# Performance work log

Measured on AMD Instinct MI355X. Metric: run time of the kernel, lower is better.

## Reference

```python
import jax, jax.numpy as jnp
import numpy as np

B, S, H, N = 2, 2048, 1024, 16
HN = H // N  # head dim = 64
EPS = 1e-12


def setup_inputs() -> dict:
    key = jax.random.key(0)
    ks = jax.random.split(key, 8)
    scale = 0.02
    return {
        "hidden_states": jax.random.normal(ks[0], (B, S, H), dtype=jnp.float32),
        "attention_mask": jnp.zeros((B, 1, 1, S), dtype=jnp.float32),
        "W_qkv": jax.random.normal(ks[1], (3 * H, H), dtype=jnp.float32) * scale,
        "b_qkv": jnp.zeros((3 * H,), dtype=jnp.float32),
        "W_out": jax.random.normal(ks[2], (H, H), dtype=jnp.float32) * scale,
        "b_out": jnp.zeros((H,), dtype=jnp.float32),
        "ln_gamma": jnp.ones((H,), dtype=jnp.float32),
        "ln_beta": jnp.zeros((H,), dtype=jnp.float32),
    }


def reference(hidden_states, attention_mask, W_qkv, b_qkv, W_out, b_out, ln_gamma, ln_beta):
    # QKV projection: torch Linear => x @ W.T + b
    qkv = jnp.einsum("bsh,oh->bso", hidden_states, W_qkv) + b_qkv  # [B,S,3H]
    q, k, v = jnp.split(qkv, 3, axis=-1)

    def heads(t):  # [B,S,H] -> [B,N,S,HN]
        return t.reshape(B, S, N, HN).transpose(0, 2, 1, 3)

    q, k, v = heads(q), heads(k), heads(v)
    nf = jnp.sqrt(jnp.sqrt(jnp.float32(HN)))
    scores = jnp.einsum("bnsd,bntd->bnst", q / nf, k / nf) + attention_mask  # [B,N,S,S]
    probs = jax.nn.softmax(scores, axis=-1)
    ctx = jnp.einsum("bnst,bntd->bnsd", probs, v)  # [B,N,S,HN]
    ctx = ctx.transpose(0, 2, 1, 3).reshape(B, S, H)

    # output dense + residual + LayerNorm
    out = jnp.einsum("bsh,oh->bso", ctx, W_out) + b_out
    x = out + hidden_states
    mean = jnp.mean(x, axis=-1, keepdims=True)
    var = jnp.mean(jnp.square(x - mean), axis=-1, keepdims=True)
    return (x - mean) * jax.lax.rsqrt(var + EPS) * ln_gamma + ln_beta
```

## Files before the change

### kernel.cpp

```cpp
#include <hip/hip_runtime.h>
#include <hip/hip_bf16.h>
#include <math.h>

#define Bq  2
#define Sq  2048
#define Hq  1024
#define Nq  16
#define HNq 64
#define Mq  (Bq*Sq)
#define H3q (3*Hq)

#define LOG2E 1.44269504088896340736f

typedef __attribute__((ext_vector_type(8))) short           short8;
typedef __attribute__((ext_vector_type(4))) short           short4s;
typedef __attribute__((ext_vector_type(8))) unsigned short  ushortx8;
typedef __attribute__((ext_vector_type(4))) unsigned short  ushortx4;
typedef __attribute__((ext_vector_type(4))) float           floatx4;

__device__ __forceinline__ unsigned short f2bf(float f) {
    union { float f; unsigned int u; } x; x.f = f;
    unsigned int r = (x.u + 0x7fffu + ((x.u >> 16) & 1u)) >> 16;
    return (unsigned short)r;
}

__device__ __forceinline__ unsigned int pkbf(float a, float b) {
    float2 t; t.x = a; t.y = b;
    __hip_bfloat162 h = __float22bfloat162_rn(t);
    union { __hip_bfloat162 h; unsigned int u; } c; c.h = h;
    return c.u;
}

__device__ __forceinline__ float bf2f(unsigned short v) {
    union { unsigned int u; float f; } x; x.u = (unsigned int)v << 16;
    return x.f;
}

__device__ __forceinline__ float fexp2(float x) {
    float r;
    asm("v_exp_f32 %0, %1" : "=v"(r) : "v"(x));
    return r;
}

__device__ __forceinline__ void gload16(const unsigned short* g, unsigned short* l) {
    __builtin_amdgcn_global_load_lds(
        (__attribute__((address_space(1))) void*)(unsigned long long)(g),
        (__attribute__((address_space(3))) void*)(unsigned int)(unsigned long long)(l),
        16, 0, 0);
}

__device__ __forceinline__ int swz(int r) { return (r ^ (r >> 2)) & 3; }

#define N_HID ((size_t)Mq * Hq)
#define N_HW  (N_HID + (size_t)H3q * Hq)
#define N_ALL (N_HW + (size_t)Hq * Hq)
#define CVT_BLKS ((int)(N_ALL / 2048))

__global__ __launch_bounds__(256) void cvt_all(
    const float* __restrict__ hidden, const float* __restrict__ wqkv,
    const float* __restrict__ wout, const float* __restrict__ mask,
    unsigned short* __restrict__ dst, unsigned short* __restrict__ em2)
{
    const int bid = blockIdx.x;
    if (bid >= CVT_BLKS) {
        const int t0   = ((bid - CVT_BLKS) * 256 + threadIdx.x) * 8;
        const int b    = t0 >> 11;
        const int t2   = t0 & 2047;
        const int kt   = t2 >> 6;
        const int t3   = t2 & 63;
        const int ks   = t3 >> 5;
        const int quad = (t3 >> 3) & 3;
        const int kb   = kt * 64 + ks * 32 + quad * 4;
        const float* mp = mask + (size_t)b * Sq + kb;
        float4 m0 = *(const float4*)(mp);
        float4 m1 = *(const float4*)(mp + 16);
        union { unsigned int u[4]; ushortx8 s; } o;
        o.u[0] = pkbf(fexp2(m0.x * LOG2E), fexp2(m0.y * LOG2E));
        o.u[1] = pkbf(fexp2(m0.z * LOG2E), fexp2(m0.w * LOG2E));
        o.u[2] = pkbf(fexp2(m1.x * LOG2E), fexp2(m1.y * LOG2E));
        o.u[3] = pkbf(fexp2(m1.z * LOG2E), fexp2(m1.w * LOG2E));
        *(ushortx8*)(em2 + t0) = o.s;
        return;
    }
    size_t i = ((size_t)bid * 256 + threadIdx.x) * 8;
    const float* src;
    if (i < N_HID)      src = hidden + i;
    else if (i < N_HW)  src = wqkv + (i - N_HID);
    else                src = wout + (i - N_HW);
    float4 a = *(const float4*)(src);
    float4 b = *(const float4*)(src + 4);
    union { unsigned int u[4]; ushortx8 s; } o;
    o.u[0] = pkbf(a.x, a.y); o.u[1] = pkbf(a.z, a.w);
    o.u[2] = pkbf(b.x, b.y); o.u[3] = pkbf(b.z, b.w);
    *(ushortx8*)(dst + i) = o.s;
}

#define TM 128
#define TN 128
#define TK 32

__global__ __launch_bounds__(256) void gemm_mfma_qkv(
    const unsigned short* __restrict__ A, const unsigned short* __restrict__ Bw,
    const float* __restrict__ bias, const float* __restrict__ mask,
    unsigned short* __restrict__ Qb, unsigned short* __restrict__ Kd,
    unsigned short* __restrict__ V5, int K)
{
    __shared__ unsigned short As[3][TM][TK];
    __shared__ unsigned short Bs[3][TN][TK];

    const int tid = threadIdx.x;
    const int w = tid >> 6, lane = tid & 63;
    const int l15 = lane & 15, quad = lane >> 4;
    const int wr = (w & 1) * 64;
    const int wc = (w >> 1) * 64;
    const int row0 = blockIdx.y * TM;
    const int col0 = blockIdx.x * TN;

    const int srow16 = lane >> 2;
    const int sgd    = lane & 3;
    const int sgsrc  = (sgd ^ swz(srow16)) * 8;

    floatx4 acc[4][4];
    #pragma unroll
    for (int i = 0; i < 4; i++)
        #pragma unroll
        for (int j = 0; j < 4; j++) acc[i][j] = (floatx4){0.f,0.f,0.f,0.f};

    const int aswz = swz(l15) * 8;
    const int NK = K / TK;

    #pragma unroll
    for (int t = 0; t < 2; t++) {
        #pragma unroll
        for (int c = 0; c < 2; c++) {
            int seg = w * 2 + c;
            int r = seg * 16 + srow16;
            gload16(A  + (size_t)(row0 + r) * K + t * TK + sgsrc, &As[t][seg * 16][0]);
            gload16(Bw + (size_t)(col0 + r) * K + t * TK + sgsrc, &Bs[t][seg * 16][0]);
        }
    }

    #pragma unroll 1
    for (int k = 0; k < NK; ++k) {
        if (k + 1 < NK) asm volatile("s_waitcnt vmcnt(4)" ::: "memory");
        else            asm volatile("s_waitcnt vmcnt(0)" ::: "memory");
        __builtin_amdgcn_s_barrier();
        __builtin_amdgcn_sched_barrier(0);

        const int cur = k % 3;
        if (k + 2 < NK) {
            const int nb  = (k + 2) % 3;
            const int k0n = (k + 2) * TK;
            #pragma unroll
            for (int c = 0; c < 2; c++) {
                int seg = w * 2 + c;
                int r = seg * 16 + srow16;
                gload16(A  + (size_t)(row0 + r) * K + k0n + sgsrc, &As[nb][seg * 16][0]);
                gload16(Bw + (size_t)(col0 + r) * K + k0n + sgsrc, &Bs[nb][seg * 16][0]);
            }
        }
        __builtin_amdgcn_sched_barrier(0);

        short8 af[4], bf[4];
        #pragma unroll
        for (int i = 0; i < 4; i++)
            af[i] = *(const short8*)&As[cur][wr + i * 16 + l15][(quad * 8) ^ aswz];
        #pragma unroll
        for (int j = 0; j < 4; j++)
            bf[j] = *(const short8*)&Bs[cur][wc + j * 16 + l15][(quad * 8) ^ aswz];
        __builtin_amdgcn_s_setprio(1);
        #pragma unroll
        for (int i = 0; i < 4; i++)
            #pragma unroll
            for (int j = 0; j < 4; j++)
                acc[i][j] = __builtin_amdgcn_mfma_f32_16x16x32_bf16(af[i], bf[j], acc[i][j], 0, 0, 0);
        __builtin_amdgcn_s_setprio(0);
    }

    const int cls = col0 >> 10;

    if (cls == 2) {
        #pragma unroll
        for (int i = 0; i < 4; i++) {
            const int rb = row0 + wr + i * 16 + quad * 4;
            const int b  = rb >> 11;
            const int s  = rb & (Sq - 1);
            const int kt32 = s >> 6;
            const int sw   = s & 63;
            const int kg   = sw >> 2;
            const int ks   = kg >> 3;
            const int q2   = kg & 3;
            const int hi   = (kg >> 2) & 1;
            float expm[4];
            #pragma unroll
            for (int rr = 0; rr < 4; rr++)
                expm[rr] = fexp2(mask[(size_t)b * Sq + s + rr] * LOG2E);
            #pragma unroll
            for (int j = 0; j < 4; j++) {
                const int c  = col0 + wc + j * 16 + l15;
                const int c2 = c - 2 * Hq;
                const int n  = c2 >> 6, d = c2 & 63;
                const int dt = d >> 4, dl = d & 15;
                const float bia = bias[c];
                ushortx4 o;
                #pragma unroll
                for (int rr = 0; rr < 4; rr++)
                    o[rr] = f2bf((acc[i][j][rr] + bia) * expm[rr]);
                const size_t off = (((size_t)(b * Nq + n) * 32 + kt32) << 12)
                                 + (size_t)((ks * 16 + dt * 4 + q2) * 128 + dl * 8 + hi * 4);
                *(ushortx4*)&V5[off] = o;
            }
        }
    } else {
        unsigned short* __restrict__ dst = (cls == 0) ? Qb : Kd;
        const int cshift = (cls == 0) ? 0 : Hq;
        const float qs = (cls == 0) ? (0.125f * LOG2E) : 1.0f;
        #pragma unroll
        for (int i = 0; i < 4; i++) {
            const int rb = row0 + wr + i * 16 + quad * 4;
            #pragma unroll
            for (int j = 0; j < 4; j++) {
                const int c = col0 + wc + j * 16 + l15;
                const float bia = bias[c];
                #pragma unroll
                for (int rr = 0; rr < 4; rr++)
                    dst[(size_t)(rb + rr) * Hq + (c - cshift)] =
                        f2bf((acc[i][j][rr] + bia) * qs);
            }
        }
    }
}

__global__ __launch_bounds__(256) void gemm_mfma_out(
    const unsigned short* __restrict__ A, const unsigned short* __restrict__ Bw,
    const float* __restrict__ bias, const float* __restrict__ res,
    unsigned short* __restrict__ X, int M, int Nd, int K)
{
    __shared__ unsigned short As[3][TM][TK];
    __shared__ unsigned short Bs[3][TN][TK];

    const int tid = threadIdx.x;
    const int w = tid >> 6, lane = tid & 63;
    const int l15 = lane & 15, quad = lane >> 4;
    const int wr = (w & 1) * 64;
    const int wc = (w >> 1) * 64;
    const int row0 = blockIdx.y * TM;
    const int col0 = blockIdx.x * TN;

    const int srow16 = lane >> 2;
    const int sgd    = lane & 3;
    const int sgsrc  = (sgd ^ swz(srow16)) * 8;

    floatx4 acc[4][4];
    #pragma unroll
    for (int i = 0; i < 4; i++)
        #pragma unroll
        for (int j = 0; j < 4; j++) acc[i][j] = (floatx4){0.f,0.f,0.f,0.f};

    const int aswz = swz(l15) * 8;
    const int NK = K / TK;

    #pragma unroll
    for (int t = 0; t < 2; t++) {
        #pragma unroll
        for (int c = 0; c < 2; c++) {
            int seg = w * 2 + c;
            int r = seg * 16 + srow16;
            gload16(A  + (size_t)(row0 + r) * K + t * TK + sgsrc, &As[t][seg * 16][0]);
            gload16(Bw + (size_t)(col0 + r) * K + t * TK + sgsrc, &Bs[t][seg * 16][0]);
        }
    }

    #pragma unroll 1
    for (int k = 0; k < NK; ++k) {
        if (k + 1 < NK) asm volatile("s_waitcnt vmcnt(4)" ::: "memory");
        else            asm volatile("s_waitcnt vmcnt(0)" ::: "memory");
        __builtin_amdgcn_s_barrier();
        __builtin_amdgcn_sched_barrier(0);

        const int cur = k % 3;
        if (k + 2 < NK) {
            const int nb  = (k + 2) % 3;
            const int k0n = (k + 2) * TK;
            #pragma unroll
            for (int c = 0; c < 2; c++) {
                int seg = w * 2 + c;
                int r = seg * 16 + srow16;
                gload16(A  + (size_t)(row0 + r) * K + k0n + sgsrc, &As[nb][seg * 16][0]);
                gload16(Bw + (size_t)(col0 + r) * K + k0n + sgsrc, &Bs[nb][seg * 16][0]);
            }
        }
        __builtin_amdgcn_sched_barrier(0);

        short8 af[4], bf[4];
        #pragma unroll
        for (int i = 0; i < 4; i++)
            af[i] = *(const short8*)&As[cur][wr + i * 16 + l15][(quad * 8) ^ aswz];
        #pragma unroll
        for (int j = 0; j < 4; j++)
            bf[j] = *(const short8*)&Bs[cur][wc + j * 16 + l15][(quad * 8) ^ aswz];
        __builtin_amdgcn_s_setprio(1);
        #pragma unroll
        for (int i = 0; i < 4; i++)
            #pragma unroll
            for (int j = 0; j < 4; j++)
                acc[i][j] = __builtin_amdgcn_mfma_f32_16x16x32_bf16(af[i], bf[j], acc[i][j], 0, 0, 0);
        __builtin_amdgcn_s_setprio(0);
    }

    #pragma unroll
    for (int i = 0; i < 4; i++) {
        const int rb = row0 + wr + i * 16 + quad * 4;
        #pragma unroll
        for (int j = 0; j < 4; j++) {
            const int c = col0 + wc + j * 16 + l15;
            const float bia = bias[c];
            #pragma unroll
            for (int rr = 0; rr < 4; rr++) {
                X[(size_t)(rb + rr) * Nd + c] =
                    f2bf(acc[i][j][rr] + bia + res[(size_t)(rb + rr) * Nd + c]);
            }
        }
    }
}

#define KTILES 16

__device__ __forceinline__ floatx4 mfma16(short8 a, short8 b, floatx4 c) {
    return __builtin_amdgcn_mfma_f32_16x16x32_bf16(a, b, c, 0, 0, 0);
}

__device__ __forceinline__ void do_lpv(
    const short8 (&pf0)[2], const short8 (&pf1)[2], const short8 (&mf)[2],
    const short8 (&vf)[8],
    floatx4 (&oacc0)[4], floatx4 (&oacc1)[4],
    floatx4 &lacc0, floatx4 &lacc1)
{
    __builtin_amdgcn_s_setprio(1);
    lacc0 = mfma16(mf[0], pf0[0], lacc0);
    lacc0 = mfma16(mf[1], pf0[1], lacc0);
    lacc1 = mfma16(mf[0], pf1[0], lacc1);
    lacc1 = mfma16(mf[1], pf1[1], lacc1);
    #pragma unroll
    for (int dt = 0; dt < 4; dt++) {
        oacc0[dt] = mfma16(vf[dt],     pf0[0], oacc0[dt]);
        oacc1[dt] = mfma16(vf[dt],     pf1[0], oacc1[dt]);
        oacc0[dt] = mfma16(vf[4 + dt], pf0[1], oacc0[dt]);
        oacc1[dt] = mfma16(vf[4 + dt], pf1[1], oacc1[dt]);
    }
    __builtin_amdgcn_s_setprio(0);
}

template<bool HAVER, bool PREF, int VWAIT>
__device__ __forceinline__ void attn_body(
    int kt,
    unsigned short (&KsL)[2][64][64],
    const unsigned short* kp, size_t kstep,
    const unsigned short* Vb, const unsigned short* e2b,
    int w, int l15, int quad,
    const short8 (&qf0)[2], const short8 (&qf1)[2],
    short8 (&vf)[8],
    const short8 (&pfR0)[2], const short8 (&pfR1)[2], const short8 (&mfR)[2],
    short8 (&pfW0)[2], short8 (&pfW1)[2], short8 (&mfW)[2],
    floatx4 (&oacc0)[4], floatx4 (&oacc1)[4],
    floatx4 &lacc0, floatx4 &lacc1)
{
    asm volatile("s_waitcnt vmcnt(%0)" :: "i"(VWAIT) : "memory");
    __builtin_amdgcn_s_barrier();
    __builtin_amdgcn_sched_barrier(0);

    const int cur = kt & 1;
    if (PREF) {
        const unsigned short* kpn = kp + (size_t)(kt + 1) * kstep;
        gload16(kpn,                  &KsL[cur ^ 1][w * 16][0]);
        gload16(kpn + (size_t)8 * Hq, &KsL[cur ^ 1][w * 16 + 8][0]);
    }
    __builtin_amdgcn_sched_barrier(0);

    const unsigned short* ep = e2b + kt * 64;
    mfW[0] = *(const short8*)(ep + quad * 8);
    mfW[1] = *(const short8*)(ep + 32 + quad * 8);

    floatx4 s0[4], s1[4];
    #pragma unroll
    for (int ct = 0; ct < 4; ct++) {
        s0[ct] = (floatx4){0.f,0.f,0.f,0.f};
        s1[ct] = (floatx4){0.f,0.f,0.f,0.f};
    }
    __builtin_amdgcn_s_setprio(1);
    #pragma unroll
    for (int ks = 0; ks < 2; ks++) {
        #pragma unroll
        for (int ct = 0; ct < 4; ct++) {
            short8 af = *(const short8*)&KsL[cur][ct * 16 + l15][((4 * ks + quad) ^ (l15 & 7)) * 8];
            s0[ct] = mfma16(af, qf0[ks], s0[ct]);
            s1[ct] = mfma16(af, qf1[ks], s1[ct]);
        }
    }
    __builtin_amdgcn_s_setprio(0);

    #pragma unroll
    for (int ks = 0; ks < 2; ks++) {
        union { unsigned int u[4]; short8 s; } pk;
        #pragma unroll
        for (int h = 0; h < 2; h++) {
            const int ct = ks * 2 + h;
            pk.u[h * 2]     = pkbf(fexp2(s0[ct][0]), fexp2(s0[ct][1]));
            pk.u[h * 2 + 1] = pkbf(fexp2(s0[ct][2]), fexp2(s0[ct][3]));
        }
        pfW0[ks] = pk.s;
    }
    #pragma unroll
    for (int ks = 0; ks < 2; ks++) {
        union { unsigned int u[4]; short8 s; } pk;
        #pragma unroll
        for (int h = 0; h < 2; h++) {
            const int ct = ks * 2 + h;
            pk.u[h * 2]     = pkbf(fexp2(s1[ct][0]), fexp2(s1[ct][1]));
            pk.u[h * 2 + 1] = pkbf(fexp2(s1[ct][2]), fexp2(s1[ct][3]));
        }
        pfW1[ks] = pk.s;
    }

    if (HAVER)
        do_lpv(pfR0, pfR1, mfR, vf, oacc0, oacc1, lacc0, lacc1);

    const unsigned short* vt = Vb + (size_t)kt * 4096 + quad * 128 + l15 * 8;
    vf[0] = *(const short8*)(vt);
    vf[1] = *(const short8*)(vt + 512);
    vf[2] = *(const short8*)(vt + 1024);
    vf[3] = *(const short8*)(vt + 1536);
    vf[4] = *(const short8*)(vt + 2048);
    vf[5] = *(const short8*)(vt + 2560);
    vf[6] = *(const short8*)(vt + 3072);
    vf[7] = *(const short8*)(vt + 3584);
}

__global__ __launch_bounds__(256) void attn_mfma(
    const unsigned short* __restrict__ Qb, const unsigned short* __restrict__ Kd,
    const unsigned short* __restrict__ V5, const unsigned short* __restrict__ em2,
    unsigned short* __restrict__ Opart, float* __restrict__ Lpart)
{
    __shared__ unsigned short Ks[2][64][64];

    const int tid  = threadIdx.x;
    const int w    = tid >> 6;
    const int lane = tid & 63;
    const int l15  = lane & 15;
    const int quad = lane >> 4;

    const int i_    = blockIdx.x;
    const int gl8   = i_ & 7;
    const int rest  = i_ >> 3;
    const int qtile = rest & 15;
    const int g     = (rest >> 4) * 8 + gl8;
    const int bn    = g >> 1;
    const int z     = g & 1;
    const int n     = bn & 15;
    const int b     = bn >> 4;

    const int kbase = z * (KTILES * 64);

    short8 qf0[2], qf1[2];
    {
        const int qrow0 = qtile * 128 + w * 16 + l15;
        const unsigned short* qp = Qb + (size_t)(b * Sq + qrow0) * Hq + n * HNq + quad * 8;
        qf0[0] = *(const short8*)(qp);
        qf0[1] = *(const short8*)(qp + 32);
        qp += (size_t)64 * Hq;
        qf1[0] = *(const short8*)(qp);
        qf1[1] = *(const short8*)(qp + 32);
    }

    floatx4 oacc0[4], oacc1[4];
    #pragma unroll
    for (int dt = 0; dt < 4; dt++) {
        oacc0[dt] = (floatx4){0.f,0.f,0.f,0.f};
        oacc1[dt] = (floatx4){0.f,0.f,0.f,0.f};
    }
    floatx4 lacc0 = (floatx4){0.f,0.f,0.f,0.f};
    floatx4 lacc1 = (floatx4){0.f,0.f,0.f,0.f};

    const int krow8 = lane >> 3;
    const int kgr   = (lane & 7) ^ (krow8 & 7);
    const unsigned short* kp = Kd + (size_t)(b * Sq + kbase + w * 16 + krow8) * Hq
                                  + n * HNq + kgr * 8;
    const size_t kstep = (size_t)64 * Hq;

    gload16(kp,                  &Ks[0][w * 16][0]);
    gload16(kp + (size_t)8 * Hq, &Ks[0][w * 16 + 8][0]);

    const unsigned short* Vb  = V5 + ((size_t)(b * Nq + n) * 32 + z * KTILES) * 4096;
    const unsigned short* e2b = em2 + (size_t)(b * 32 + z * KTILES) * 64;

    short8 vf[8];
    short8 pfA0[2], pfA1[2], mfA[2];
    short8 pfB0[2], pfB1[2], mfB[2];

    attn_body<false, true, 0>(0, Ks, kp, kstep, Vb, e2b, w, l15, quad,
        qf0, qf1, vf, pfB0, pfB1, mfB, pfA0, pfA1, mfA, oacc0, oacc1, lacc0, lacc1);

    #pragma unroll 1
    for (int kt = 1; kt < KTILES - 1; kt += 2) {
        attn_body<true, true, 10>(kt, Ks, kp, kstep, Vb, e2b, w, l15, quad,
            qf0, qf1, vf, pfA0, pfA1, mfA, pfB0, pfB1, mfB, oacc0, oacc1, lacc0, lacc1);
        attn_body<true, true, 10>(kt + 1, Ks, kp, kstep, Vb, e2b, w, l15, quad,
            qf0, qf1, vf, pfB0, pfB1, mfB, pfA0, pfA1, mfA, oacc0, oacc1, lacc0, lacc1);
    }
    attn_body<true, false, 10>(KTILES - 1, Ks, kp, kstep, Vb, e2b, w, l15, quad,
        qf0, qf1, vf, pfA0, pfA1, mfA, pfB0, pfB1, mfB, oacc0, oacc1, lacc0, lacc1);
    do_lpv(pfB0, pfB1, mfB, vf, oacc0, oacc1, lacc0, lacc1);

    unsigned short* Ow = Opart + (size_t)z * Mq * Hq;
    #pragma unroll
    for (int sub = 0; sub < 2; sub++) {
        const float l_i = sub ? lacc1[0] : lacc0[0];
        const int qrow = qtile * 128 + sub * 64 + w * 16 + l15;
        if (quad == 0)
            Lpart[(size_t)z * Mq * Nq + (size_t)(b * Sq + qrow) * Nq + n] = l_i;
        #pragma unroll
        for (int dt = 0; dt < 4; dt++) {
            const floatx4 oa = sub ? oacc1[dt] : oacc0[dt];
            union { unsigned int u[2]; ushortx4 s; } o;
            o.u[0] = pkbf(oa[0], oa[1]);
            o.u[1] = pkbf(oa[2], oa[3]);
            const int col = n * HNq + dt * 16 + quad * 4;
            *(ushortx4*)&Ow[(size_t)(b * Sq + qrow) * Hq + col] = o.s;
        }
    }
}

__global__ __launch_bounds__(256) void attn_merge(
    const unsigned short* __restrict__ Opart, const float* __restrict__ Lpart,
    unsigned short* __restrict__ ctx)
{
    const size_t idx = ((size_t)blockIdx.x * 256 + threadIdx.x) * 4;
    const int row = (int)(idx >> 10);
    const int n   = ((int)idx >> 6) & 15;
    const float l = Lpart[(size_t)row * Nq + n]
                  + Lpart[(size_t)Mq * Nq + (size_t)row * Nq + n];
    const float inv = 1.0f / l;
    ushortx4 a = *(const ushortx4*)(Opart + idx);
    ushortx4 c = *(const ushortx4*)(Opart + (size_t)Mq * Hq + idx);
    union { unsigned int u[2]; ushortx4 s; } o;
    o.u[0] = pkbf((bf2f(a[0]) + bf2f(c[0])) * inv, (bf2f(a[1]) + bf2f(c[1])) * inv);
    o.u[1] = pkbf((bf2f(a[2]) + bf2f(c[2])) * inv, (bf2f(a[3]) + bf2f(c[3])) * inv);
    *(ushortx4*)(ctx + idx) = o.s;
}

__global__ __launch_bounds__(256) void ln_kernel(
    const unsigned short* __restrict__ X, const float* __restrict__ gamma,
    const float* __restrict__ beta, float* __restrict__ out)
{
    const int row = blockIdx.x;
    const int c0  = threadIdx.x * 4;
    ushortx4 xv = *(const ushortx4*)(X + (size_t)row * Hq + c0);
    float vals[4];
    float lsum = 0.0f;
    #pragma unroll
    for (int i = 0; i < 4; i++) { vals[i] = bf2f(xv[i]); lsum += vals[i]; }

    __shared__ float red[8];
    const int wid = threadIdx.x >> 6, lane = threadIdx.x & 63;

    float s = lsum;
    #pragma unroll
    for (int off = 32; off >= 1; off >>= 1) s += __shfl_xor(s, off, 64);
    if (lane == 0) red[wid] = s;
    __syncthreads();
    const float mean = (red[0] + red[1] + red[2] + red[3]) * (1.0f / Hq);

    float v = 0.0f;
    #pragma unroll
    for (int i = 0; i < 4; i++) { float d = vals[i] - mean; v += d * d; }
    #pragma unroll
    for (int off = 32; off >= 1; off >>= 1) v += __shfl_xor(v, off, 64);
    if (lane == 0) red[4 + wid] = v;
    __syncthreads();
    const float var  = (red[4] + red[5] + red[6] + red[7]) * (1.0f / Hq);
    const float rstd = rsqrtf(var + 1e-12f);

    float4 gm = *(const float4*)(gamma + c0);
    float4 bt = *(const float4*)(beta + c0);
    float4 o;
    o.x = (vals[0] - mean) * rstd * gm.x + bt.x;
    o.y = (vals[1] - mean) * rstd * gm.y + bt.y;
    o.z = (vals[2] - mean) * rstd * gm.z + bt.z;
    o.w = (vals[3] - mean) * rstd * gm.w + bt.w;
    *(float4*)(out + (size_t)row * Hq + c0) = o;
}

extern "C" void kernel_launch(void* const* d_in, const int* in_sizes, int n_in,
                              void* d_out, int out_size, void* d_ws, size_t ws_size,
                              hipStream_t stream)
{
    const float* hidden = (const float*)d_in[0];
    const float* mask   = (const float*)d_in[1];
    const float* W_qkv  = (const float*)d_in[2];
    const float* b_qkv  = (const float*)d_in[3];
    const float* W_out  = (const float*)d_in[4];
    const float* b_out  = (const float*)d_in[5];
    const float* gamma  = (const float*)d_in[6];
    const float* beta   = (const float*)d_in[7];
    float* out = (float*)d_out;

    const size_t nHid  = (size_t)Mq * Hq;
    const size_t nWq   = (size_t)H3q * Hq;
    const size_t nWo   = (size_t)Hq * Hq;
    const size_t nCtx  = (size_t)Mq * Hq;

    unsigned short* hidden_bf = (unsigned short*)d_ws;
    unsigned short* Wqkv_bf   = hidden_bf + nHid;
    unsigned short* Wout_bf   = Wqkv_bf + nWq;
    unsigned short* qb        = Wout_bf + nWo;
    unsigned short* kd        = qb + nHid;
    unsigned short* v5        = kd + nHid;
    unsigned short* ctx_bf    = v5 + nHid;
    unsigned short* x_bf      = ctx_bf + nCtx;
    unsigned short* opart     = x_bf + nHid;
    float*          lpart     = (float*)(opart + 2 * nHid);
    unsigned short* em2       = (unsigned short*)(lpart + 2 * (size_t)Mq * Nq);

    dim3 blk(256);

    cvt_all<<<dim3(CVT_BLKS + 2), blk, 0, stream>>>(
        hidden, W_qkv, W_out, mask, hidden_bf, em2);

    gemm_mfma_qkv<<<dim3(H3q / TN, Mq / TM), blk, 0, stream>>>(
        hidden_bf, Wqkv_bf, b_qkv, mask, qb, kd, v5, Hq);

    attn_mfma<<<dim3(1024), blk, 0, stream>>>(
        qb, kd, v5, em2, opart, lpart);

    attn_merge<<<dim3((int)(nCtx / 1024)), blk, 0, stream>>>(
        opart, lpart, ctx_bf);

    gemm_mfma_out<<<dim3(Hq / TN, Mq / TM), blk, 0, stream>>>(
        ctx_bf, Wout_bf, b_out, hidden, x_bf, Mq, Hq, Hq);

    ln_kernel<<<dim3(Mq), blk, 0, stream>>>(x_bf, gamma, beta, out);
}
```

Measured before the change: 203.5 us.

## Stage V tiles through triple-buffered LDS instead of direct global register loads

New measurement: 203.3 us. About the same (-0.1%).

```diff
diff --git a/kernel.cpp b/kernel.cpp
--- a/kernel.cpp
+++ b/kernel.cpp
@@ -332,7 +332,7 @@
 
 __device__ __forceinline__ void do_lpv(
     const short8 (&pf0)[2], const short8 (&pf1)[2], const short8 (&mf)[2],
-    const short8 (&vf)[8],
+    const unsigned short* Vt,
     floatx4 (&oacc0)[4], floatx4 (&oacc1)[4],
     floatx4 &lacc0, floatx4 &lacc1)
 {
@@ -343,37 +343,42 @@
     lacc1 = mfma16(mf[1], pf1[1], lacc1);
     #pragma unroll
     for (int dt = 0; dt < 4; dt++) {
-        oacc0[dt] = mfma16(vf[dt],     pf0[0], oacc0[dt]);
-        oacc1[dt] = mfma16(vf[dt],     pf1[0], oacc1[dt]);
-        oacc0[dt] = mfma16(vf[4 + dt], pf0[1], oacc0[dt]);
-        oacc1[dt] = mfma16(vf[4 + dt], pf1[1], oacc1[dt]);
+        short8 vlo = *(const short8*)(Vt + dt * 512);
+        short8 vhi = *(const short8*)(Vt + 2048 + dt * 512);
+        oacc0[dt] = mfma16(vlo, pf0[0], oacc0[dt]);
+        oacc1[dt] = mfma16(vlo, pf1[0], oacc1[dt]);
+        oacc0[dt] = mfma16(vhi, pf0[1], oacc0[dt]);
+        oacc1[dt] = mfma16(vhi, pf1[1], oacc1[dt]);
     }
     __builtin_amdgcn_s_setprio(0);
 }
 
-template<bool HAVER, bool PREF, int VWAIT>
+template<bool HAVER, bool PREF>
 __device__ __forceinline__ void attn_body(
     int kt,
     unsigned short (&KsL)[2][64][64],
+    unsigned short (&VsL)[3][4096],
     const unsigned short* kp, size_t kstep,
     const unsigned short* Vb, const unsigned short* e2b,
-    int w, int l15, int quad,
+    int w, int l15, int quad, int lane,
     const short8 (&qf0)[2], const short8 (&qf1)[2],
-    short8 (&vf)[8],
     const short8 (&pfR0)[2], const short8 (&pfR1)[2], const short8 (&mfR)[2],
     short8 (&pfW0)[2], short8 (&pfW1)[2], short8 (&mfW)[2],
     floatx4 (&oacc0)[4], floatx4 (&oacc1)[4],
     floatx4 &lacc0, floatx4 &lacc1)
 {
-    asm volatile("s_waitcnt vmcnt(%0)" :: "i"(VWAIT) : "memory");
+    asm volatile("s_waitcnt vmcnt(0)" ::: "memory");
     __builtin_amdgcn_s_barrier();
     __builtin_amdgcn_sched_barrier(0);
 
-    const int cur = kt & 1;
     if (PREF) {
         const unsigned short* kpn = kp + (size_t)(kt + 1) * kstep;
-        gload16(kpn,                  &KsL[cur ^ 1][w * 16][0]);
-        gload16(kpn + (size_t)8 * Hq, &KsL[cur ^ 1][w * 16 + 8][0]);
+        gload16(kpn,                  &KsL[(kt + 1) & 1][w * 16][0]);
+        gload16(kpn + (size_t)8 * Hq, &KsL[(kt + 1) & 1][w * 16 + 8][0]);
+        const unsigned short* vpn = Vb + (size_t)(kt + 1) * 4096 + w * 1024 + lane * 8;
+        unsigned short* vd = &VsL[(kt + 1) % 3][w * 1024];
+        gload16(vpn,       vd);
+        gload16(vpn + 512, vd + 512);
     }
     __builtin_amdgcn_sched_barrier(0);
 
@@ -392,7 +397,7 @@
     for (int ks = 0; ks < 2; ks++) {
         #pragma unroll
         for (int ct = 0; ct < 4; ct++) {
-            short8 af = *(const short8*)&KsL[cur][ct * 16 + l15][((4 * ks + quad) ^ (l15 & 7)) * 8];
+            short8 af = *(const short8*)&KsL[kt & 1][ct * 16 + l15][((4 * ks + quad) ^ (l15 & 7)) * 8];
             s0[ct] = mfma16(af, qf0[ks], s0[ct]);
             s1[ct] = mfma16(af, qf1[ks], s1[ct]);
         }
@@ -423,17 +428,8 @@
     }
 
     if (HAVER)
-        do_lpv(pfR0, pfR1, mfR, vf, oacc0, oacc1, lacc0, lacc1);
-
-    const unsigned short* vt = Vb + (size_t)kt * 4096 + quad * 128 + l15 * 8;
-    vf[0] = *(const short8*)(vt);
-    vf[1] = *(const short8*)(vt + 512);
-    vf[2] = *(const short8*)(vt + 1024);
-    vf[3] = *(const short8*)(vt + 1536);
-    vf[4] = *(const short8*)(vt + 2048);
-    vf[5] = *(const short8*)(vt + 2560);
-    vf[6] = *(const short8*)(vt + 3072);
-    vf[7] = *(const short8*)(vt + 3584);
+        do_lpv(pfR0, pfR1, mfR, &VsL[(kt - 1) % 3][0] + lane * 8,
+               oacc0, oacc1, lacc0, lacc1);
 }
 
 __global__ __launch_bounds__(256) void attn_mfma(
@@ -442,6 +438,7 @@
     unsigned short* __restrict__ Opart, float* __restrict__ Lpart)
 {
     __shared__ unsigned short Ks[2][64][64];
+    __shared__ unsigned short Vs[3][4096];
 
     const int tid  = threadIdx.x;
     const int w    = tid >> 6;
@@ -487,29 +484,34 @@
                                   + n * HNq + kgr * 8;
     const size_t kstep = (size_t)64 * Hq;
 
+    const unsigned short* Vb  = V5 + ((size_t)(b * Nq + n) * 32 + z * KTILES) * 4096;
+    const unsigned short* e2b = em2 + (size_t)(b * 32 + z * KTILES) * 64;
+
     gload16(kp,                  &Ks[0][w * 16][0]);
     gload16(kp + (size_t)8 * Hq, &Ks[0][w * 16 + 8][0]);
-
-    const unsigned short* Vb  = V5 + ((size_t)(b * Nq + n) * 32 + z * KTILES) * 4096;
-    const unsigned short* e2b = em2 + (size_t)(b * 32 + z * KTILES) * 64;
-
-    short8 vf[8];
+    {
+        const unsigned short* vp0 = Vb + w * 1024 + lane * 8;
+        gload16(vp0,       &Vs[0][w * 1024]);
+        gload16(vp0 + 512, &Vs[0][w * 1024] + 512);
+    }
+
     short8 pfA0[2], pfA1[2], mfA[2];
     short8 pfB0[2], pfB1[2], mfB[2];
 
-    attn_body<false, true, 0>(0, Ks, kp, kstep, Vb, e2b, w, l15, quad,
-        qf0, qf1, vf, pfB0, pfB1, mfB, pfA0, pfA1, mfA, oacc0, oacc1, lacc0, lacc1);
+    attn_body<false, true>(0, Ks, Vs, kp, kstep, Vb, e2b, w, l15, quad, lane,
+        qf0, qf1, pfB0, pfB1, mfB, pfA0, pfA1, mfA, oacc0, oacc1, lacc0, lacc1);
 
     #pragma unroll 1
     for (int kt = 1; kt < KTILES - 1; kt += 2) {
-        attn_body<true, true, 10>(kt, Ks, kp, kstep, Vb, e2b, w, l15, quad,
-            qf0, qf1, vf, pfA0, pfA1, mfA, pfB0, pfB1, mfB, oacc0, oacc1, lacc0, lacc1);
-        attn_body<true, true, 10>(kt + 1, Ks, kp, kstep, Vb, e2b, w, l15, quad,
-            qf0, qf1, vf, pfB0, pfB1, mfB, pfA0, pfA1, mfA, oacc0, oacc1, lacc0, lacc1);
-    }
-    attn_body<true, false, 10>(KTILES - 1, Ks, kp, kstep, Vb, e2b, w, l15, quad,
-        qf0, qf1, vf, pfA0, pfA1, mfA, pfB0, pfB1, mfB, oacc0, oacc1, lacc0, lacc1);
-    do_lpv(pfB0, pfB1, mfB, vf, oacc0, oacc1, lacc0, lacc1);
+        attn_body<true, true>(kt, Ks, Vs, kp, kstep, Vb, e2b, w, l15, quad, lane,
+            qf0, qf1, pfA0, pfA1, mfA, pfB0, pfB1, mfB, oacc0, oacc1, lacc0, lacc1);
+        attn_body<true, true>(kt + 1, Ks, Vs, kp, kstep, Vb, e2b, w, l15, quad, lane,
+            qf0, qf1, pfB0, pfB1, mfB, pfA0, pfA1, mfA, oacc0, oacc1, lacc0, lacc1);
+    }
+    attn_body<true, false>(KTILES - 1, Ks, Vs, kp, kstep, Vb, e2b, w, l15, quad, lane,
+        qf0, qf1, pfA0, pfA1, mfA, pfB0, pfB1, mfB, oacc0, oacc1, lacc0, lacc1);
+    do_lpv(pfB0, pfB1, mfB, &Vs[(KTILES - 1) % 3][0] + lane * 8,
+           oacc0, oacc1, lacc0, lacc1);
 
     unsigned short* Ow = Opart + (size_t)z * Mq * Hq;
     #pragma unroll
```
